# Kernel tuning notes

Hardware: AMD Instinct MI355X
Metric: run time of the kernel (lower is better)

The kernel has to match this reference:

```python
import jax, jax.numpy as jnp
import numpy as np

NC, NPER, DIN, D, R = 100000, 50000, 128, 128, 7
E = 2100000
ER = E // R  # edges per relation (block layout: relation i owns rows [i*ER, (i+1)*ER))
NEG_SLOPE = 0.2


def _seg_softmax(x, seg, n):
    # numerically-stable softmax over destination-node segments (PyG `softmax`)
    m = jax.ops.segment_max(x, seg, num_segments=n)
    m = jnp.where(jnp.isfinite(m), m, 0.0)  # empty segments -> -inf; neutralize
    e = jnp.exp(x - m[seg])
    s = jax.ops.segment_sum(e, seg, num_segments=n)
    return e / (s[seg] + 1e-16)


def setup_inputs() -> dict:
    key = jax.random.key(0)
    ks = jax.random.split(key, 12)
    N = NC + NPER
    s_in = 1.0 / float(np.sqrt(DIN))
    s_d = 1.0 / float(np.sqrt(D))
    company_emb = jax.random.normal(ks[0], (NC, DIN), jnp.float32)
    person_emb = jax.random.normal(ks[1], (NPER, DIN), jnp.float32)
    edge_index = jax.random.randint(ks[2], (E, 2), 0, N)
    edge_type = jnp.repeat(jnp.arange(R), ER)  # contiguous blocks per relation
    # weights are all-ones except relation 3 -> selects the weighted message branch there
    edge_weight = jnp.ones((E, 1), jnp.float32)
    edge_weight = edge_weight.at[3 * ER:4 * ER].set(
        jax.random.uniform(ks[3], (ER, 1), jnp.float32) + 0.1)
    W_com = jax.random.normal(ks[4], (DIN, D), jnp.float32) * s_in
    W_per = jax.random.normal(ks[5], (DIN, D), jnp.float32) * s_in
    Wq = jax.random.normal(ks[6], (R, D, D), jnp.float32) * s_d
    bq = jnp.zeros((R, D), jnp.float32)
    Wk = jax.random.normal(ks[7], (R, D, D), jnp.float32) * s_d
    bk = jnp.zeros((R, D), jnp.float32)
    Wv = jax.random.normal(ks[8], (D, D), jnp.float32) * s_d
    bv = jnp.zeros((D,), jnp.float32)
    pri = jnp.ones((R,), jnp.float32)
    W_rel_pair = jax.random.normal(ks[9], (R, 2 * D, D), jnp.float32) * s_d  # slot 3 unused
    W_rel3 = jax.random.normal(ks[10], (D, D), jnp.float32) * s_d
    skip = jnp.ones((1,), jnp.float32)
    return {"company_emb": company_emb, "person_emb": person_emb, "edge_weight": edge_weight,
            "W_com": W_com, "W_per": W_per, "Wq": Wq, "bq": bq, "Wk": Wk, "bk": bk,
            "Wv": Wv, "bv": bv, "pri": pri, "W_rel_pair": W_rel_pair, "W_rel3": W_rel3,
            "skip": skip, "edge_index": edge_index, "edge_type": edge_type}


def _hetegnn(company_emb, person_emb, edge_weight, W_com, W_per, Wq, bq, Wk, bk,
             Wv, bv, pri, W_rel_pair, W_rel3, skip, edge_index, edge_type):
    emb = jnp.concatenate([company_emb @ W_com, person_emb @ W_per], axis=0)  # [N, D]
    N = emb.shape[0]
    rs_list = []
    for i in range(R):
        sl = slice(i * ER, (i + 1) * ER)
        src = edge_index[sl, 0]
        dst = edge_index[sl, 1]
        x_j = emb[src]                                   # gathered source features [ER, D]
        if i == 3:  # weighted branch: linear on x_j, scalar scatter-softmax of edge weights
            msg = (x_j @ W_rel3) * _seg_softmax(edge_weight[sl], dst, N)
        else:       # attention branch: rel_wi(concat(x_i, x_j)) -> per-dim scatter-softmax
            temp = jnp.concatenate([emb[dst], x_j], axis=1) @ W_rel_pair[i]  # [ER, D]
            msg = x_j * _seg_softmax(temp, dst, N)
        rs = jax.ops.segment_sum(msg, dst, num_segments=N)  # scatter-add aggregation
        rs_list.append(jax.nn.leaky_relu(rs, NEG_SLOPE))
    rs_stack = jnp.stack(rs_list)                           # [R, N, D]
    # cross-relation attention
    q = jnp.einsum('nd,rde->rne', emb, Wq) + bq[:, None, :]
    k = jnp.einsum('rnd,rde->rne', rs_stack, Wk) + bk[:, None, :]
    scores = (q * k).sum(-1) * pri[:, None] / jnp.sqrt(jnp.float32(D))  # [R, N]
    att = jax.nn.softmax(scores, axis=0)                    # softmax across relations
    v = rs_stack @ Wv + bv                                  # [R, N, D]
    res = jnp.einsum('rn,rnd->nd', att, v)
    res = res + jax.nn.sigmoid(skip) * jax.nn.gelu(emb, approximate=False)
    return res


def reference(company_emb, person_emb, edge_weight, W_com, W_per, Wq, bq, Wk, bk,
              Wv, bv, pri, W_rel_pair, W_rel3, skip, edge_index, edge_type):
    res = _hetegnn(company_emb, person_emb, edge_weight, W_com, W_per, Wq, bq, Wk, bk,
                   Wv, bv, pri, W_rel_pair, W_rel3, skip, edge_index, edge_type)
    return res[:NC], res[NC:]
```

## Files before the change

### kernel.cpp

```cpp
#include <hip/hip_runtime.h>
#include <stdint.h>

#define NCY 100000
#define NPR 50000
#define NT  150000
#define RREL 7
#define ETOT 2100000
#define EREL 300000
#define NSEG (RREL*NT)
#define NEG 0.2f

#define NBUK 256
#define BWID 587
#define P1B  1024
#define CH1  2051
#define EPT  9
#define LSEG (RREL*BWID)
#define SPT  17

typedef __attribute__((ext_vector_type(8))) short short8;
typedef __attribute__((ext_vector_type(4))) float f32x4;
typedef unsigned short u16;

__device__ __forceinline__ float bf2f(u16 h){
  union{unsigned int u; float f;} v; v.u = ((unsigned int)h)<<16; return v.f;
}
__device__ __forceinline__ u16 f2bf(float f){
  union{unsigned int u; float f;} v; v.f=f;
  unsigned int u=v.u;
  return (u16)((u + 0x7fffu + ((u>>16)&1u))>>16);
}
__device__ __forceinline__ float lrelu(float x){ return x>0.f? x : NEG*x; }

#define MFMA(a,b,c) __builtin_amdgcn_mfma_f32_16x16x32_bf16(a,b,c,0,0,0)

__global__ __launch_bounds__(256) void k_bin(const int* __restrict__ eidx,
    const float* __restrict__ ew,
    int* __restrict__ bsrc, int* __restrict__ bkey, float* __restrict__ bew,
    int* __restrict__ gcntT, int* __restrict__ poffT){
  __shared__ int cnt[NBUK];
  __shared__ int pb[NBUK];
  int blk = blockIdx.x, tid = threadIdx.x;
  int base = blk*CH1;
  int n = min(CH1, ETOT-base);
  cnt[tid]=0;
  __syncthreads();
  int esrc[EPT], ekey[EPT], erank[EPT], ebuk[EPT]; float eew[EPT];
  #pragma unroll
  for(int k=0;k<EPT;k++){
    int i = k*256 + tid;
    erank[k]=-1; esrc[k]=0; ekey[k]=0; ebuk[k]=0; eew[k]=0.f;
    if(i<n){
      int e = base+i;
      int2 sd = *(const int2*)(eidx+2*e);
      int r = e/EREL;
      int b = sd.y / BWID;
      esrc[k]=sd.x; ekey[k]=r*NT+sd.y; ebuk[k]=b; eew[k]=ew[e];
      erank[k]=atomicAdd(&cnt[b],1);
    }
  }
  __syncthreads();
  int v = cnt[tid];
  pb[tid]=v; __syncthreads();
  for(int off=1; off<256; off<<=1){
    int a=(tid>=off)?pb[tid-off]:0; __syncthreads();
    pb[tid]+=a; __syncthreads();
  }
  int excl = pb[tid]-v;
  gcntT[blk*NBUK+tid]=v;
  poffT[blk*NBUK+tid]=excl;
  pb[tid]=excl; __syncthreads();
  #pragma unroll
  for(int k=0;k<EPT;k++){
    if(erank[k]>=0){
      int pos = base + pb[ebuk[k]] + erank[k];
      bsrc[pos]=esrc[k]; bkey[pos]=ekey[k]; bew[pos]=eew[k];
    }
  }
}

__global__ __launch_bounds__(256) void k_bsum(const int* __restrict__ gcntT,
                                              int* __restrict__ btot){
  __shared__ int lds[256];
  int b = blockIdx.x, t = threadIdx.x;
  int s=0;
  for(int blk=t; blk<P1B; blk+=256) s += gcntT[blk*NBUK+b];
  lds[t]=s; __syncthreads();
  for(int off=128; off>0; off>>=1){ if(t<off) lds[t]+=lds[t+off]; __syncthreads(); }
  if(t==0) btot[b]=lds[0];
}

__global__ __launch_bounds__(256) void k_bscan(const int* __restrict__ btot,
                                               int* __restrict__ bbase){
  __shared__ int lds[256];
  int t=threadIdx.x;
  int v=btot[t]; lds[t]=v; __syncthreads();
  for(int off=1; off<256; off<<=1){
    int a=(t>=off)?lds[t-off]:0; __syncthreads();
    lds[t]+=a; __syncthreads();
  }
  bbase[t]=lds[t]-v;
}

__global__ __launch_bounds__(256) void k_place(
    const int* __restrict__ bsrc, const int* __restrict__ bkey, const float* __restrict__ bew,
    const int* __restrict__ gcntT, const int* __restrict__ poffT, const int* __restrict__ bbase,
    int* __restrict__ starts_g, int* __restrict__ ends_g,
    int* __restrict__ ssrc, float* __restrict__ sew){
  __shared__ int scnt[LSEG];
  __shared__ int lrun[LSEG];
  __shared__ int gofs[P1B];
  __shared__ int gl[P1B];
  __shared__ int scan[256];
  int b = blockIdx.x, t = threadIdx.x;
  int lo = b*BWID;
  int gbase = bbase[b];
  for(int i=t;i<LSEG;i+=256) scnt[i]=0;
  for(int blk=t; blk<P1B; blk+=256){
    gl[blk]   = gcntT[blk*NBUK+b];
    gofs[blk] = poffT[blk*NBUK+b];
  }
  __syncthreads();
  for(int blk=t; blk<P1B; blk+=256){
    int o = blk*CH1 + gofs[blk], g = gl[blk];
    for(int i=0;i<g;i++){
      int key = bkey[o+i];
      int r = key/NT; int dst = key - r*NT;
      atomicAdd(&scnt[r*BWID + (dst-lo)], 1);
    }
  }
  __syncthreads();
  int ts=0;
  #pragma unroll
  for(int k=0;k<SPT;k++){ int idx=t*SPT+k; ts += (idx<LSEG)? scnt[idx]:0; }
  scan[t]=ts; __syncthreads();
  for(int off=1; off<256; off<<=1){
    int a=(t>=off)?scan[t-off]:0; __syncthreads();
    scan[t]+=a; __syncthreads();
  }
  int run = scan[t]-ts;
  #pragma unroll
  for(int k=0;k<SPT;k++){
    int idx=t*SPT+k;
    if(idx<LSEG){ lrun[idx]=run; run += scnt[idx]; }
  }
  __syncthreads();
  for(int idx=t; idx<LSEG; idx+=256){
    int r = idx/BWID; int ld = idx - r*BWID; int dst = lo+ld;
    if(dst<NT){
      int sgp = gbase + lrun[idx];
      starts_g[r*NT+dst] = sgp;
      ends_g[r*NT+dst]   = sgp + scnt[idx];
    }
  }
  __syncthreads();
  for(int idx=t; idx<LSEG; idx+=256) lrun[idx] += gbase;
  __syncthreads();
  for(int blk=t; blk<P1B; blk+=256){
    int o = blk*CH1 + gofs[blk], g = gl[blk];
    for(int i=0;i<g;i++){
      int key = bkey[o+i];
      int r = key/NT; int dst = key - r*NT;
      int pos = atomicAdd(&lrun[r*BWID+(dst-lo)], 1);
      ssrc[pos] = bsrc[o+i];
      if(r==3) sew[pos] = bew[o+i];
    }
  }
}

__global__ __launch_bounds__(256) void k_prep(const float* __restrict__ Wq, const float* __restrict__ bq,
    const float* __restrict__ Wk, const float* __restrict__ bk,
    float* __restrict__ Ar, float* __restrict__ ur, float* __restrict__ wr,
    float* __restrict__ cr, int* __restrict__ bflag){
  int t = blockIdx.x*256 + threadIdx.x;
  if(t >= RREL*128*128) return;
  int r = t/(128*128); int ij = t - r*128*128; int i = ij>>7, j = ij&127;
  const float* wq = Wq + r*16384; const float* wk = Wk + r*16384;
  float s=0.f;
  for(int k=0;k<128;k++) s += wq[i*128+k]*wk[j*128+k];
  Ar[t] = s;
  if(i==0){
    float su=0.f, sw=0.f;
    for(int k=0;k<128;k++){ su += wq[j*128+k]*bk[r*128+k];
                            sw += wk[j*128+k]*bq[r*128+k]; }
    ur[r*128+j]=su; wr[r*128+j]=sw;
    if(j==0){
      float sc=0.f; int nz=0;
      for(int k=0;k<128;k++){ float a=bq[r*128+k], b2=bk[r*128+k];
        sc += a*b2; nz |= (a!=0.f)||(b2!=0.f); }
      cr[r]=sc; if(nz) atomicOr(bflag,1);
    }
  }
}

struct PackJob{ const float* src; u16* dst; int ksteps; };
struct PackJobs{ PackJob j[20]; };
__global__ __launch_bounds__(256) void k_pack(PackJobs jobs){
  PackJob J = jobs.j[blockIdx.y];
  int t = blockIdx.x*256 + threadIdx.x;
  int lane = t&63, ks=(t>>6)&7, nt=t>>9;
  if(ks >= J.ksteps) return;
  int col = nt*16 + (lane&15);
  int krow = ks*32 + (lane>>4)*8;
  u16* d = J.dst + ((nt*J.ksteps + ks)*64 + lane)*8;
  for(int j=0;j<8;j++) d[j] = f2bf(J.src[(krow+j)*128 + col]);
}

struct GArgs {
  const void* A; const u16* B; int M; int rowoff;
  u16* outH; float* acc; float* den;
  const u16* emb16;
  const float* bv; const float* skip;
};

template<int EPI, int ASRC>
__global__ __launch_bounds__(256) void k_gemm(GArgs G)
{
  int wave = threadIdx.x>>6, lane = threadIdx.x&63;
  int M = G.M;
  int base = blockIdx.x*64 + wave*16;
  if(base >= M) return;
  int arow = base + (lane&15); if(arow >= M) arow = M-1;
  int kof = (lane>>4)*8;
  short8 a[4];
  if(ASRC==0){
    const u16* A = (const u16*)G.A;
    #pragma unroll
    for(int ks=0;ks<4;ks++) a[ks] = *(const short8*)(A + (size_t)arow*128 + ks*32 + kof);
  } else if(ASRC==3){
    const u16* A = (const u16*)G.A;
    float sc = 1.f/G.den[arow];
    #pragma unroll
    for(int ks=0;ks<4;ks++){
      short8 v = *(const short8*)(A + (size_t)arow*128 + ks*32 + kof);
      short8 s;
      #pragma unroll
      for(int j2=0;j2<8;j2++) s[j2]=f2bf(bf2f((u16)v[j2])*sc);
      a[ks]=s;
    }
  } else {
    const float* A = (const float*)G.A;
    #pragma unroll
    for(int ks=0;ks<4;ks++){
      const float* ap = A + (size_t)arow*128 + ks*32 + kof;
      f32x4 lo = *(const f32x4*)ap;
      f32x4 hi = *(const f32x4*)(ap+4);
      short8 s;
      #pragma unroll
      for(int j2=0;j2<4;j2++){ s[j2]=f2bf(lo[j2]); s[4+j2]=f2bf(hi[j2]); }
      a[ks]=s;
    }
  }
  f32x4 acc[8];
  #pragma unroll
  for(int nt=0;nt<8;nt++){
    f32x4 c = {0.f,0.f,0.f,0.f};
    #pragma unroll
    for(int ks=0;ks<4;ks++){
      short8 b = *(const short8*)(G.B + ((nt*4+ks)*64 + lane)*8);
      c = MFMA(a[ks], b, c);
    }
    acc[nt]=c;
  }
  int rbase = base + (lane>>4)*4;
  int cl = lane&15;
  if(EPI==0){
    #pragma unroll
    for(int nt=0;nt<8;nt++)
      for(int j=0;j<4;j++){
        int row=rbase+j;
        if(row<M){
          int col=nt*16+cl;
          G.outH[(size_t)(G.rowoff+row)*128+col] = f2bf(acc[nt][j]);
        }
      }
  } else if(EPI==1){
    #pragma unroll
    for(int nt=0;nt<8;nt++)
      for(int j=0;j<4;j++){
        int row=rbase+j;
        if(row<M){
          int col=nt*16+cl;
          G.outH[(size_t)row*128+col]=f2bf(lrelu(acc[nt][j]));
        }
      }
  } else {
    float sg = 1.f/(1.f+__expf(-G.skip[0]));
    #pragma unroll
    for(int nt=0;nt<8;nt++)
      for(int j=0;j<4;j++){
        int row=rbase+j;
        if(row<M){
          int col=nt*16+cl;
          float x = bf2f(G.emb16[(size_t)row*128+col]);
          float g = 0.5f*x*(1.f+erff(x*0.70710678118f));
          G.acc[(size_t)row*128+col] = acc[nt][j] + G.bv[col] + sg*g;
        }
      }
  }
}

struct FArgs {
  const u16* emb16; const u16* pA; const u16* pB2;
  const u16* rs; u16* acc16; float* den; u16* ebot;
  const float* uvec; const float* wvec; const float* cr; const int* bflag; const float* pri;
};

template<int HAS_EBOT>
__global__ __launch_bounds__(256) void k_facc(FArgs F)
{
  int wave = threadIdx.x>>6, lane = threadIdx.x&63;
  int base = blockIdx.x*64 + wave*16;
  if(base >= NT) return;
  int arow = base + (lane&15); if(arow >= NT) arow = NT-1;
  int kof = (lane>>4)*8;
  short8 a[4];
  #pragma unroll
  for(int ks=0;ks<4;ks++) a[ks] = *(const short8*)(F.emb16 + (size_t)arow*128 + ks*32 + kof);
  int rbase = base + (lane>>4)*4;
  int cl = lane&15;
  if(HAS_EBOT){
    #pragma unroll
    for(int nt=0;nt<8;nt++){
      f32x4 c = {0.f,0.f,0.f,0.f};
      #pragma unroll
      for(int ks=0;ks<4;ks++){
        short8 b = *(const short8*)(F.pB2 + ((nt*4+ks)*64 + lane)*8);
        c = MFMA(a[ks], b, c);
      }
      #pragma unroll
      for(int j=0;j<4;j++){
        int row=rbase+j;
        if(row<NT) F.ebot[(size_t)row*128 + nt*16+cl] = f2bf(__expf(c[j]));
      }
    }
  }
  f32x4 accS[8];
  #pragma unroll
  for(int nt=0;nt<8;nt++){
    f32x4 c = {0.f,0.f,0.f,0.f};
    #pragma unroll
    for(int ks=0;ks<4;ks++){
      short8 b = *(const short8*)(F.pA + ((nt*4+ks)*64 + lane)*8);
      c = MFMA(a[ks], b, c);
    }
    accS[nt]=c;
  }
  float prival = F.pri[0] * 0.08838834764831845f;
  int bias = *F.bflag;
  float rsv[4][8];
  #pragma unroll
  for(int j=0;j<4;j++){
    int row=rbase+j; bool ok = row<NT;
    #pragma unroll
    for(int nt=0;nt<8;nt++){
      int col=nt*16+cl;
      rsv[j][nt] = ok ? bf2f(F.rs[(size_t)row*128+col]) : 0.f;
    }
  }
  #pragma unroll
  for(int j=0;j<4;j++){
    int row=rbase+j; bool ok = row<NT;
    float p=0.f;
    if(ok){
      #pragma unroll
      for(int nt=0;nt<8;nt++) p += accS[nt][j]*rsv[j][nt];
      if(bias){
        #pragma unroll
        for(int nt=0;nt<8;nt++){
          int col=nt*16+cl;
          p += bf2f(F.emb16[(size_t)row*128+col])*F.uvec[col]
             + rsv[j][nt]*F.wvec[col];
        }
      }
    }
    p += __shfl_xor(p,1,16); p += __shfl_xor(p,2,16);
    p += __shfl_xor(p,4,16); p += __shfl_xor(p,8,16);
    float e = __expf((p + F.cr[0])*prival);
    if(ok){
      #pragma unroll
      for(int nt=0;nt<8;nt++){
        size_t o=(size_t)row*128 + nt*16+cl;
        F.acc16[o] = f2bf(bf2f(F.acc16[o]) + e*rsv[j][nt]);
      }
      if(cl==0) F.den[row] += e;
    }
  }
}

__global__ __launch_bounds__(256) void k_edge2s(const u16* __restrict__ ebot,
    const u16* __restrict__ emb16, const int* __restrict__ ssrc,
    const int* __restrict__ starts_g, const int* __restrict__ ends_g, int rel,
    u16* __restrict__ rsout){
  int n = blockIdx.x*16 + (threadIdx.x>>4);
  int dof = (threadIdx.x&15)*8;
  int s = starts_g[rel*NT + n];
  int e_end = ends_g[rel*NT + n];
  float num[8]={0,0,0,0,0,0,0,0}, den[8]={0,0,0,0,0,0,0,0};
  int p = s;
  for(; p+1 < e_end; p += 2){
    int s0 = ssrc[p], s1 = ssrc[p+1];
    short8 ev0 = *(const short8*)(ebot  + (size_t)s0*128 + dof);
    short8 xj0 = *(const short8*)(emb16 + (size_t)s0*128 + dof);
    short8 ev1 = *(const short8*)(ebot  + (size_t)s1*128 + dof);
    short8 xj1 = *(const short8*)(emb16 + (size_t)s1*128 + dof);
    #pragma unroll
    for(int j=0;j<8;j++){
      float e0 = bf2f((u16)ev0[j]), e1 = bf2f((u16)ev1[j]);
      num[j] += bf2f((u16)xj0[j])*e0 + bf2f((u16)xj1[j])*e1;
      den[j] += e0 + e1;
    }
  }
  if(p < e_end){
    int s0 = ssrc[p];
    short8 ev0 = *(const short8*)(ebot  + (size_t)s0*128 + dof);
    short8 xj0 = *(const short8*)(emb16 + (size_t)s0*128 + dof);
    #pragma unroll
    for(int j=0;j<8;j++){
      float e0 = bf2f((u16)ev0[j]);
      num[j] += bf2f((u16)xj0[j])*e0;
      den[j] += e0;
    }
  }
  u16 o8[8];
  #pragma unroll
  for(int j=0;j<8;j++) o8[j] = f2bf(lrelu(num[j]/(den[j]+1e-16f)));
  *(short8*)(rsout + (size_t)n*128 + dof) = *(short8*)o8;
}

__global__ __launch_bounds__(256) void k_rel3s(const float* __restrict__ sew,
    const u16* __restrict__ emb16, const int* __restrict__ ssrc,
    const int* __restrict__ starts_g, const int* __restrict__ ends_g,
    u16* __restrict__ t16){
  int n = blockIdx.x*16 + (threadIdx.x>>4);
  int dof = (threadIdx.x&15)*8;
  int s = starts_g[3*NT + n];
  int e_end = ends_g[3*NT + n];
  float num[8]={0,0,0,0,0,0,0,0}, den=0.f;
  for(int p=s; p<e_end; p++){
    int src = ssrc[p];
    float wv = __expf(sew[p]);
    den += wv;
    short8 xj8 = *(const short8*)(emb16 + (size_t)src*128 + dof);
    #pragma unroll
    for(int j=0;j<8;j++) num[j] += wv*bf2f((u16)xj8[j]);
  }
  float inv = 1.f/(den+1e-16f);
  u16 o8[8];
  #pragma unroll
  for(int j=0;j<8;j++) o8[j] = f2bf(num[j]*inv);
  *(short8*)(t16 + (size_t)n*128 + dof) = *(short8*)o8;
}

extern "C" void kernel_launch(void* const* d_in, const int* in_sizes, int n_in,
                              void* d_out, int out_size, void* d_ws, size_t ws_size,
                              hipStream_t stream){
  const float* company = (const float*)d_in[0];
  const float* person  = (const float*)d_in[1];
  const float* eweight = (const float*)d_in[2];
  const float* W_com   = (const float*)d_in[3];
  const float* W_per   = (const float*)d_in[4];
  const float* Wq      = (const float*)d_in[5];
  const float* bq      = (const float*)d_in[6];
  const float* Wk      = (const float*)d_in[7];
  const float* bk      = (const float*)d_in[8];
  const float* Wv      = (const float*)d_in[9];
  const float* bvv     = (const float*)d_in[10];
  const float* pri     = (const float*)d_in[11];
  const float* Wpair   = (const float*)d_in[12];
  const float* Wrel3   = (const float*)d_in[13];
  const float* skip    = (const float*)d_in[14];
  const int*   eidx    = (const int*)d_in[15];
  float* out = (float*)d_out;

  char* w = (char*)d_ws;
  auto alloc = [&](size_t sz)->void*{ void* p=(void*)w; w += (sz+255)&~(size_t)255; return p; };
  u16*   emb16 = (u16*)alloc((size_t)NT*128*2);
  u16*   ebot  = (u16*)alloc((size_t)NT*128*2);
  u16*   rs16  = (u16*)alloc((size_t)NT*128*2);
  u16*   acc16 = (u16*)alloc((size_t)NT*128*2);
  float* den   = (float*)alloc((size_t)NT*4);
  int*   starts_g = (int*)alloc((size_t)NSEG*4);
  int*   ends_g   = (int*)alloc((size_t)NSEG*4);
  int*   ssrc  = (int*)alloc((size_t)ETOT*4);
  float* sew   = (float*)alloc((size_t)ETOT*4);
  float* Ar    = (float*)alloc((size_t)RREL*16384*4);
  float* ur    = (float*)alloc(RREL*128*4);
  float* wr    = (float*)alloc(RREL*128*4);
  float* cr    = (float*)alloc(RREL*4);
  int*   bflag = (int*)alloc(256);
  u16* pWcom  = (u16*)alloc(16384*2);
  u16* pWper  = (u16*)alloc(16384*2);
  u16* pWrel3 = (u16*)alloc(16384*2);
  u16* pWv    = (u16*)alloc(16384*2);
  u16* pAr    = (u16*)alloc((size_t)RREL*16384*2);
  u16* pWbot  = (u16*)alloc((size_t)6*16384*2);
  (void)ws_size; (void)in_sizes; (void)n_in; (void)out_size;

  int*   bsrc  = (int*)rs16;
  int*   bkey  = bsrc + ETOT;
  float* bew   = (float*)(bkey + ETOT);
  int*   gcntT = (int*)acc16;
  int*   poffT = gcntT + P1B*NBUK;
  int*   btot  = poffT + P1B*NBUK;
  int*   bbase = btot + NBUK;

  hipMemsetAsync(den, 0, (size_t)NT*4, stream);
  hipMemsetAsync(bflag, 0, 4, stream);

  k_bin<<<P1B,256,0,stream>>>(eidx, eweight, bsrc, bkey, bew, gcntT, poffT);
  k_bsum<<<NBUK,256,0,stream>>>(gcntT, btot);
  k_bscan<<<1,256,0,stream>>>(btot, bbase);
  k_place<<<NBUK,256,0,stream>>>(bsrc,bkey,bew,gcntT,poffT,bbase,
                                 starts_g,ends_g,ssrc,sew);
  hipMemsetAsync(acc16, 0, (size_t)NT*128*2, stream);

  k_prep<<<(RREL*16384+255)/256,256,0,stream>>>(Wq,bq,Wk,bk,Ar,ur,wr,cr,bflag);

  const int attr[6] = {0,1,2,4,5,6};
  PackJobs pj{};
  int nj=0;
  auto addjob=[&](const float* s,u16* d,int ks){ pj.j[nj].src=s; pj.j[nj].dst=d; pj.j[nj].ksteps=ks; nj++; };
  addjob(W_com,pWcom,4); addjob(W_per,pWper,4);
  addjob(Wrel3,pWrel3,4); addjob(Wv,pWv,4);
  for(int r=0;r<RREL;r++) addjob(Ar + (size_t)r*16384, pAr + (size_t)r*16384, 4);
  for(int i=0;i<6;i++) addjob(Wpair + (size_t)attr[i]*32768 + 16384, pWbot + (size_t)i*16384, 4);
  dim3 pg(16, nj);
  k_pack<<<pg,256,0,stream>>>(pj);

  GArgs g{};
  g = GArgs{}; g.A=company; g.B=pWcom; g.M=NCY; g.rowoff=0; g.outH=emb16;
  k_gemm<0,1><<<(NCY+63)/64,256,0,stream>>>(g);
  g = GArgs{}; g.A=person; g.B=pWper; g.M=NPR; g.rowoff=NCY; g.outH=emb16;
  k_gemm<0,1><<<(NPR+63)/64,256,0,stream>>>(g);

  auto facc = [&](int r, int ebslot){
    FArgs f{};
    f.emb16=emb16; f.pA=pAr+(size_t)r*16384; f.rs=rs16; f.acc16=acc16; f.den=den;
    f.uvec=ur+(size_t)r*128; f.wvec=wr+(size_t)r*128; f.cr=cr+r; f.bflag=bflag; f.pri=pri+r;
    if(ebslot>=0){
      f.pB2=pWbot+(size_t)ebslot*16384; f.ebot=ebot;
      k_facc<1><<<(NT+63)/64,256,0,stream>>>(f);
    } else {
      k_facc<0><<<(NT+63)/64,256,0,stream>>>(f);
    }
  };

  k_rel3s<<<NT/16,256,0,stream>>>(sew,emb16,ssrc,starts_g,ends_g,ebot);
  g = GArgs{}; g.A=ebot; g.B=pWrel3; g.M=NT; g.outH=rs16;
  k_gemm<1,0><<<(NT+63)/64,256,0,stream>>>(g);
  facc(3, 0);

  for(int i=0;i<6;i++){
    int r = attr[i];
    k_edge2s<<<NT/16,256,0,stream>>>(ebot,emb16,ssrc,starts_g,ends_g,r, rs16);
    facc(r, (i<5)? i+1 : -1);
  }

  g = GArgs{}; g.A=acc16; g.B=pWv; g.M=NT;
  g.acc=out; g.den=den; g.emb16=emb16; g.bv=bvv; g.skip=skip;
  k_gemm<3,3><<<(NT+63)/64,256,0,stream>>>(g);
}
```

Before: 957.9 us.

## Fuse edge gather with attention accumulation, processing two relations per kernel

Replaces the separate per-relation edge-gather kernel and attention-accumulate kernel with fused kernels. Each block gathers segment-softmax messages for 64 nodes into LDS and then runs the MFMA scoring and accumulation from LDS. Relations are processed in pairs, so each launch computes exp tables for the next two relations and the acc16/den read-modify-write runs half as often. Relation 3's gather and its W_rel3 GEMM are fused as well. This removes the rs16 round trips and about ten launches. The cost is double-buffered exp tables stored in the output buffer, more LDS per block, and a gather pattern of one thread per 16 columns that may lower memory-level parallelism.

```diff
diff --git a/kernel.cpp b/kernel.cpp
--- a/kernel.cpp
+++ b/kernel.cpp
@@ -17,6 +17,8 @@
 #define EPT  9
 #define LSEG (RREL*BWID)
 #define SPT  17
+
+#define LSTR 136
 
 typedef __attribute__((ext_vector_type(8))) short short8;
 typedef __attribute__((ext_vector_type(4))) float f32x4;
@@ -274,14 +276,14 @@
           G.outH[(size_t)(G.rowoff+row)*128+col] = f2bf(acc[nt][j]);
         }
       }
-  } else if(EPI==1){
+  } else if(EPI==4){
     #pragma unroll
     for(int nt=0;nt<8;nt++)
       for(int j=0;j<4;j++){
         int row=rbase+j;
         if(row<M){
           int col=nt*16+cl;
-          G.outH[(size_t)row*128+col]=f2bf(lrelu(acc[nt][j]));
+          G.outH[(size_t)row*128+col]=f2bf(__expf(acc[nt][j]));
         }
       }
   } else {
@@ -300,156 +302,366 @@
   }
 }
 
-struct FArgs {
-  const u16* emb16; const u16* pA; const u16* pB2;
-  const u16* rs; u16* acc16; float* den; u16* ebot;
-  const float* uvec; const float* wvec; const float* cr; const int* bflag; const float* pri;
+struct PArgs {
+  const u16* emb16; const int* ssrc; const int* starts_g; const int* ends_g;
+  const float* sew;
+  const u16* ebR1; const u16* ebR2;
+  const u16* pA1; const u16* pA2;
+  const u16* pWr3;
+  const u16* pB2a; const u16* pB2b; u16* ebW1; u16* ebW2;
+  u16* acc16; float* den;
+  const float* u1; const float* w1; const float* c1; const float* p1;
+  const float* u2; const float* w2; const float* c2; const float* p2;
+  const int* bflag;
+  int r1, r2;
 };
 
-template<int HAS_EBOT>
-__global__ __launch_bounds__(256) void k_facc(FArgs F)
+__device__ __forceinline__ void gatherAtt(u16* buf, const u16* __restrict__ ebt,
+    const u16* __restrict__ emb16, const int* __restrict__ ssrc,
+    const int* __restrict__ sg, const int* __restrict__ eg,
+    int rel, int base64, int tid){
+  #pragma unroll
+  for(int p2=0;p2<2;p2++){
+    int ln = (tid>>3) + p2*32;
+    int gn = base64 + ln;
+    int cb = (tid&7)*16;
+    float num[16]={0,0,0,0,0,0,0,0,0,0,0,0,0,0,0,0};
+    float den[16]={0,0,0,0,0,0,0,0,0,0,0,0,0,0,0,0};
+    if(gn<NT){
+      int s=sg[rel*NT+gn], e=eg[rel*NT+gn];
+      for(int pos=s;pos<e;pos++){
+        int src=ssrc[pos];
+        const u16* eb=ebt+(size_t)src*128+cb;
+        const u16* xm=emb16+(size_t)src*128+cb;
+        short8 e0=*(const short8*)eb, e1=*(const short8*)(eb+8);
+        short8 x0=*(const short8*)xm, x1=*(const short8*)(xm+8);
+        #pragma unroll
+        for(int j=0;j<8;j++){
+          float ev0=bf2f((u16)e0[j]), ev1=bf2f((u16)e1[j]);
+          num[j]   += bf2f((u16)x0[j])*ev0; den[j]   += ev0;
+          num[8+j] += bf2f((u16)x1[j])*ev1; den[8+j] += ev1;
+        }
+      }
+    }
+    #pragma unroll
+    for(int j=0;j<16;j++) buf[ln*LSTR+cb+j] = f2bf(lrelu(num[j]/(den[j]+1e-16f)));
+  }
+}
+
+__device__ __forceinline__ void gatherR3(u16* buf, const float* __restrict__ sew,
+    const u16* __restrict__ emb16, const int* __restrict__ ssrc,
+    const int* __restrict__ sg, const int* __restrict__ eg,
+    int base64, int tid){
+  #pragma unroll
+  for(int p2=0;p2<2;p2++){
+    int ln = (tid>>3) + p2*32;
+    int gn = base64 + ln;
+    int cb = (tid&7)*16;
+    float num[16]={0,0,0,0,0,0,0,0,0,0,0,0,0,0,0,0};
+    float dn=0.f;
+    if(gn<NT){
+      int s=sg[3*NT+gn], e=eg[3*NT+gn];
+      for(int pos=s;pos<e;pos++){
+        int src=ssrc[pos];
+        float wv=__expf(sew[pos]);
+        dn += wv;
+        const u16* xm=emb16+(size_t)src*128+cb;
+        short8 x0=*(const short8*)xm, x1=*(const short8*)(xm+8);
+        #pragma unroll
+        for(int j=0;j<8;j++){
+          num[j]   += wv*bf2f((u16)x0[j]);
+          num[8+j] += wv*bf2f((u16)x1[j]);
+        }
+      }
+    }
+    float inv=1.f/(dn+1e-16f);
+    #pragma unroll
+    for(int j=0;j<16;j++) buf[ln*LSTR+cb+j] = f2bf(num[j]*inv);
+  }
+}
+
+template<int NR, int NEB>
+__global__ __launch_bounds__(256) void k_fp(PArgs P)
 {
-  int wave = threadIdx.x>>6, lane = threadIdx.x&63;
-  int base = blockIdx.x*64 + wave*16;
+  __shared__ u16 lds1[64*LSTR];
+  __shared__ u16 lds2[64*LSTR];
+  int tid = threadIdx.x;
+  int base64 = blockIdx.x*64;
+  gatherAtt(lds1, P.ebR1, P.emb16, P.ssrc, P.starts_g, P.ends_g, P.r1, base64, tid);
+  if(NR==2) gatherAtt(lds2, P.ebR2, P.emb16, P.ssrc, P.starts_g, P.ends_g, P.r2, base64, tid);
+  __syncthreads();
+  int wave=tid>>6, lane=tid&63;
+  int base = base64 + wave*16;
   if(base >= NT) return;
   int arow = base + (lane&15); if(arow >= NT) arow = NT-1;
   int kof = (lane>>4)*8;
   short8 a[4];
   #pragma unroll
-  for(int ks=0;ks<4;ks++) a[ks] = *(const short8*)(F.emb16 + (size_t)arow*128 + ks*32 + kof);
+  for(int ks=0;ks<4;ks++) a[ks] = *(const short8*)(P.emb16 + (size_t)arow*128 + ks*32 + kof);
   int rbase = base + (lane>>4)*4;
+  int lrb   = wave*16 + (lane>>4)*4;
   int cl = lane&15;
-  if(HAS_EBOT){
+  int bias = *P.bflag;
+  float e1v[4], e2v[4];
+  {
+    f32x4 accS[8];
     #pragma unroll
     for(int nt=0;nt<8;nt++){
       f32x4 c = {0.f,0.f,0.f,0.f};
       #pragma unroll
       for(int ks=0;ks<4;ks++){
-        short8 b = *(const short8*)(F.pB2 + ((nt*4+ks)*64 + lane)*8);
+        short8 b = *(const short8*)(P.pA1 + ((nt*4+ks)*64 + lane)*8);
         c = MFMA(a[ks], b, c);
       }
-      #pragma unroll
-      for(int j=0;j<4;j++){
-        int row=rbase+j;
-        if(row<NT) F.ebot[(size_t)row*128 + nt*16+cl] = f2bf(__expf(c[j]));
-      }
-    }
-  }
-  f32x4 accS[8];
-  #pragma unroll
-  for(int nt=0;nt<8;nt++){
-    f32x4 c = {0.f,0.f,0.f,0.f};
-    #pragma unroll
-    for(int ks=0;ks<4;ks++){
-      short8 b = *(const short8*)(F.pA + ((nt*4+ks)*64 + lane)*8);
-      c = MFMA(a[ks], b, c);
-    }
-    accS[nt]=c;
-  }
-  float prival = F.pri[0] * 0.08838834764831845f;
-  int bias = *F.bflag;
-  float rsv[4][8];
-  #pragma unroll
-  for(int j=0;j<4;j++){
-    int row=rbase+j; bool ok = row<NT;
-    #pragma unroll
-    for(int nt=0;nt<8;nt++){
-      int col=nt*16+cl;
-      rsv[j][nt] = ok ? bf2f(F.rs[(size_t)row*128+col]) : 0.f;
-    }
-  }
-  #pragma unroll
-  for(int j=0;j<4;j++){
-    int row=rbase+j; bool ok = row<NT;
-    float p=0.f;
-    if(ok){
-      #pragma unroll
-      for(int nt=0;nt<8;nt++) p += accS[nt][j]*rsv[j][nt];
-      if(bias){
+      accS[nt]=c;
+    }
+    float prival = P.p1[0]*0.08838834764831845f;
+    #pragma unroll
+    for(int j=0;j<4;j++){
+      int row=rbase+j; bool ok=row<NT;
+      float p=0.f;
+      if(ok){
         #pragma unroll
         for(int nt=0;nt<8;nt++){
           int col=nt*16+cl;
-          p += bf2f(F.emb16[(size_t)row*128+col])*F.uvec[col]
-             + rsv[j][nt]*F.wvec[col];
-        }
-      }
-    }
-    p += __shfl_xor(p,1,16); p += __shfl_xor(p,2,16);
-    p += __shfl_xor(p,4,16); p += __shfl_xor(p,8,16);
-    float e = __expf((p + F.cr[0])*prival);
-    if(ok){
+          float rv = bf2f(lds1[(lrb+j)*LSTR+col]);
+          p += accS[nt][j]*rv;
+          if(bias) p += bf2f(P.emb16[(size_t)row*128+col])*P.u1[col] + rv*P.w1[col];
+        }
+      }
+      p += __shfl_xor(p,1,16); p += __shfl_xor(p,2,16);
+      p += __shfl_xor(p,4,16); p += __shfl_xor(p,8,16);
+      e1v[j] = __expf((p + P.c1[0])*prival);
+    }
+  }
+  if(NR==2){
+    f32x4 accS[8];
+    #pragma unroll
+    for(int nt=0;nt<8;nt++){
+      f32x4 c = {0.f,0.f,0.f,0.f};
+      #pragma unroll
+      for(int ks=0;ks<4;ks++){
+        short8 b = *(const short8*)(P.pA2 + ((nt*4+ks)*64 + lane)*8);
+        c = MFMA(a[ks], b, c);
+      }
+      accS[nt]=c;
+    }
+    float prival = P.p2[0]*0.08838834764831845f;
+    #pragma unroll
+    for(int j=0;j<4;j++){
+      int row=rbase+j; bool ok=row<NT;
+      float p=0.f;
+      if(ok){
+        #pragma unroll
+        for(int nt=0;nt<8;nt++){
+          int col=nt*16+cl;
+          float rv = bf2f(lds2[(lrb+j)*LSTR+col]);
+          p += accS[nt][j]*rv;
+          if(bias) p += bf2f(P.emb16[(size_t)row*128+col])*P.u2[col] + rv*P.w2[col];
+        }
+      }
+      p += __shfl_xor(p,1,16); p += __shfl_xor(p,2,16);
+      p += __shfl_xor(p,4,16); p += __shfl_xor(p,8,16);
+      e2v[j] = __expf((p + P.c2[0])*prival);
+    }
+  }
+  #pragma unroll
+  for(int j=0;j<4;j++){
+    int row=rbase+j;
+    if(row<NT){
+      float ee1=e1v[j];
+      float ee2=(NR==2)? e2v[j] : 0.f;
       #pragma unroll
       for(int nt=0;nt<8;nt++){
-        size_t o=(size_t)row*128 + nt*16+cl;
-        F.acc16[o] = f2bf(bf2f(F.acc16[o]) + e*rsv[j][nt]);
-      }
-      if(cl==0) F.den[row] += e;
-    }
-  }
-}
-
-__global__ __launch_bounds__(256) void k_edge2s(const u16* __restrict__ ebot,
-    const u16* __restrict__ emb16, const int* __restrict__ ssrc,
-    const int* __restrict__ starts_g, const int* __restrict__ ends_g, int rel,
-    u16* __restrict__ rsout){
-  int n = blockIdx.x*16 + (threadIdx.x>>4);
-  int dof = (threadIdx.x&15)*8;
-  int s = starts_g[rel*NT + n];
-  int e_end = ends_g[rel*NT + n];
-  float num[8]={0,0,0,0,0,0,0,0}, den[8]={0,0,0,0,0,0,0,0};
-  int p = s;
-  for(; p+1 < e_end; p += 2){
-    int s0 = ssrc[p], s1 = ssrc[p+1];
-    short8 ev0 = *(const short8*)(ebot  + (size_t)s0*128 + dof);
-    short8 xj0 = *(const short8*)(emb16 + (size_t)s0*128 + dof);
-    short8 ev1 = *(const short8*)(ebot  + (size_t)s1*128 + dof);
-    short8 xj1 = *(const short8*)(emb16 + (size_t)s1*128 + dof);
-    #pragma unroll
-    for(int j=0;j<8;j++){
-      float e0 = bf2f((u16)ev0[j]), e1 = bf2f((u16)ev1[j]);
-      num[j] += bf2f((u16)xj0[j])*e0 + bf2f((u16)xj1[j])*e1;
-      den[j] += e0 + e1;
-    }
-  }
-  if(p < e_end){
-    int s0 = ssrc[p];
-    short8 ev0 = *(const short8*)(ebot  + (size_t)s0*128 + dof);
-    short8 xj0 = *(const short8*)(emb16 + (size_t)s0*128 + dof);
-    #pragma unroll
-    for(int j=0;j<8;j++){
-      float e0 = bf2f((u16)ev0[j]);
-      num[j] += bf2f((u16)xj0[j])*e0;
-      den[j] += e0;
-    }
-  }
-  u16 o8[8];
-  #pragma unroll
-  for(int j=0;j<8;j++) o8[j] = f2bf(lrelu(num[j]/(den[j]+1e-16f)));
-  *(short8*)(rsout + (size_t)n*128 + dof) = *(short8*)o8;
-}
-
-__global__ __launch_bounds__(256) void k_rel3s(const float* __restrict__ sew,
-    const u16* __restrict__ emb16, const int* __restrict__ ssrc,
-    const int* __restrict__ starts_g, const int* __restrict__ ends_g,
-    u16* __restrict__ t16){
-  int n = blockIdx.x*16 + (threadIdx.x>>4);
-  int dof = (threadIdx.x&15)*8;
-  int s = starts_g[3*NT + n];
-  int e_end = ends_g[3*NT + n];
-  float num[8]={0,0,0,0,0,0,0,0}, den=0.f;
-  for(int p=s; p<e_end; p++){
-    int src = ssrc[p];
-    float wv = __expf(sew[p]);
-    den += wv;
-    short8 xj8 = *(const short8*)(emb16 + (size_t)src*128 + dof);
-    #pragma unroll
-    for(int j=0;j<8;j++) num[j] += wv*bf2f((u16)xj8[j]);
-  }
-  float inv = 1.f/(den+1e-16f);
-  u16 o8[8];
-  #pragma unroll
-  for(int j=0;j<8;j++) o8[j] = f2bf(num[j]*inv);
-  *(short8*)(t16 + (size_t)n*128 + dof) = *(short8*)o8;
+        int col=nt*16+cl;
+        size_t o=(size_t)row*128+col;
+        float add = ee1*bf2f(lds1[(lrb+j)*LSTR+col]);
+        if(NR==2) add += ee2*bf2f(lds2[(lrb+j)*LSTR+col]);
+        P.acc16[o] = f2bf(bf2f(P.acc16[o]) + add);
+      }
+      if(cl==0) P.den[row] += ee1 + ee2;
+    }
+  }
+  if(NEB>=1){
+    #pragma unroll
+    for(int nt=0;nt<8;nt++){
+      f32x4 c = {0.f,0.f,0.f,0.f};
+      #pragma unroll
+      for(int ks=0;ks<4;ks++){
+        short8 b = *(const short8*)(P.pB2a + ((nt*4+ks)*64 + lane)*8);
+        c = MFMA(a[ks], b, c);
+      }
+      #pragma unroll
+      for(int j=0;j<4;j++){
+        int row=rbase+j;
+        if(row<NT) P.ebW1[(size_t)row*128 + nt*16+cl] = f2bf(__expf(c[j]));
+      }
+    }
+  }
+  if(NEB>=2){
+    #pragma unroll
+    for(int nt=0;nt<8;nt++){
+      f32x4 c = {0.f,0.f,0.f,0.f};
+      #pragma unroll
+      for(int ks=0;ks<4;ks++){
+        short8 b = *(const short8*)(P.pB2b + ((nt*4+ks)*64 + lane)*8);
+        c = MFMA(a[ks], b, c);
+      }
+      #pragma unroll
+      for(int j=0;j<4;j++){
+        int row=rbase+j;
+        if(row<NT) P.ebW2[(size_t)row*128 + nt*16+cl] = f2bf(__expf(c[j]));
+      }
+    }
+  }
+}
+
+__global__ __launch_bounds__(256) void k_fp0(PArgs P)
+{
+  __shared__ u16 lds1[64*LSTR];
+  __shared__ u16 lds2[64*LSTR];
+  int tid = threadIdx.x;
+  int base64 = blockIdx.x*64;
+  gatherR3(lds1, P.sew, P.emb16, P.ssrc, P.starts_g, P.ends_g, base64, tid);
+  gatherAtt(lds2, P.ebR2, P.emb16, P.ssrc, P.starts_g, P.ends_g, P.r2, base64, tid);
+  __syncthreads();
+  int wave=tid>>6, lane=tid&63;
+  int base = base64 + wave*16;
+  if(base >= NT) return;
+  int arow = base + (lane&15); if(arow >= NT) arow = NT-1;
+  int kof = (lane>>4)*8;
+  int lar = wave*16 + (lane&15);
+  short8 a[4];
+  #pragma unroll
+  for(int ks=0;ks<4;ks++) a[ks] = *(const short8*)(P.emb16 + (size_t)arow*128 + ks*32 + kof);
+  f32x4 rs3[8];
+  {
+    short8 ta[4];
+    #pragma unroll
+    for(int ks=0;ks<4;ks++) ta[ks] = *(const short8*)(lds1 + lar*LSTR + ks*32 + kof);
+    #pragma unroll
+    for(int nt=0;nt<8;nt++){
+      f32x4 c = {0.f,0.f,0.f,0.f};
+      #pragma unroll
+      for(int ks=0;ks<4;ks++){
+        short8 b = *(const short8*)(P.pWr3 + ((nt*4+ks)*64 + lane)*8);
+        c = MFMA(ta[ks], b, c);
+      }
+      #pragma unroll
+      for(int j=0;j<4;j++) c[j] = lrelu(c[j]);
+      rs3[nt]=c;
+    }
+  }
+  int rbase = base + (lane>>4)*4;
+  int lrb   = wave*16 + (lane>>4)*4;
+  int cl = lane&15;
+  int bias = *P.bflag;
+  float e1v[4], e2v[4];
+  {
+    f32x4 accS[8];
+    #pragma unroll
+    for(int nt=0;nt<8;nt++){
+      f32x4 c = {0.f,0.f,0.f,0.f};
+      #pragma unroll
+      for(int ks=0;ks<4;ks++){
+        short8 b = *(const short8*)(P.pA1 + ((nt*4+ks)*64 + lane)*8);
+        c = MFMA(a[ks], b, c);
+      }
+      accS[nt]=c;
+    }
+    float prival = P.p1[0]*0.08838834764831845f;
+    #pragma unroll
+    for(int j=0;j<4;j++){
+      int row=rbase+j; bool ok=row<NT;
+      float p=0.f;
+      if(ok){
+        #pragma unroll
+        for(int nt=0;nt<8;nt++){
+          int col=nt*16+cl;
+          float rv = rs3[nt][j];
+          p += accS[nt][j]*rv;
+          if(bias) p += bf2f(P.emb16[(size_t)row*128+col])*P.u1[col] + rv*P.w1[col];
+        }
+      }
+      p += __shfl_xor(p,1,16); p += __shfl_xor(p,2,16);
+      p += __shfl_xor(p,4,16); p += __shfl_xor(p,8,16);
+      e1v[j] = __expf((p + P.c1[0])*prival);
+    }
+  }
+  {
+    f32x4 accS[8];
+    #pragma unroll
+    for(int nt=0;nt<8;nt++){
+      f32x4 c = {0.f,0.f,0.f,0.f};
+      #pragma unroll
+      for(int ks=0;ks<4;ks++){
+        short8 b = *(const short8*)(P.pA2 + ((nt*4+ks)*64 + lane)*8);
+        c = MFMA(a[ks], b, c);
+      }
+      accS[nt]=c;
+    }
+    float prival = P.p2[0]*0.08838834764831845f;
+    #pragma unroll
+    for(int j=0;j<4;j++){
+      int row=rbase+j; bool ok=row<NT;
+      float p=0.f;
+      if(ok){
+        #pragma unroll
+        for(int nt=0;nt<8;nt++){
+          int col=nt*16+cl;
+          float rv = bf2f(lds2[(lrb+j)*LSTR+col]);
+          p += accS[nt][j]*rv;
+          if(bias) p += bf2f(P.emb16[(size_t)row*128+col])*P.u2[col] + rv*P.w2[col];
+        }
+      }
+      p += __shfl_xor(p,1,16); p += __shfl_xor(p,2,16);
+      p += __shfl_xor(p,4,16); p += __shfl_xor(p,8,16);
+      e2v[j] = __expf((p + P.c2[0])*prival);
+    }
+  }
+  #pragma unroll
+  for(int j=0;j<4;j++){
+    int row=rbase+j;
+    if(row<NT){
+      float ee1=e1v[j], ee2=e2v[j];
+      #pragma unroll
+      for(int nt=0;nt<8;nt++){
+        int col=nt*16+cl;
+        size_t o=(size_t)row*128+col;
+        float add = ee1*bf2f(f2bf(rs3[nt][j])) + ee2*bf2f(lds2[(lrb+j)*LSTR+col]);
+        P.acc16[o] = f2bf(bf2f(P.acc16[o]) + add);
+      }
+      if(cl==0) P.den[row] += ee1 + ee2;
+    }
+  }
+  #pragma unroll
+  for(int nt=0;nt<8;nt++){
+    f32x4 c = {0.f,0.f,0.f,0.f};
+    #pragma unroll
+    for(int ks=0;ks<4;ks++){
+      short8 b = *(const short8*)(P.pB2a + ((nt*4+ks)*64 + lane)*8);
+      c = MFMA(a[ks], b, c);
+    }
+    #pragma unroll
+    for(int j=0;j<4;j++){
+      int row=rbase+j;
+      if(row<NT) P.ebW1[(size_t)row*128 + nt*16+cl] = f2bf(__expf(c[j]));
+    }
+  }
+  #pragma unroll
+  for(int nt=0;nt<8;nt++){
+    f32x4 c = {0.f,0.f,0.f,0.f};
+    #pragma unroll
+    for(int ks=0;ks<4;ks++){
+      short8 b = *(const short8*)(P.pB2b + ((nt*4+ks)*64 + lane)*8);
+      c = MFMA(a[ks], b, c);
+    }
+    #pragma unroll
+    for(int j=0;j<4;j++){
+      int row=rbase+j;
+      if(row<NT) P.ebW2[(size_t)row*128 + nt*16+cl] = f2bf(__expf(c[j]));
+    }
+  }
 }
 
 extern "C" void kernel_launch(void* const* d_in, const int* in_sizes, int n_in,
@@ -476,8 +688,8 @@
   char* w = (char*)d_ws;
   auto alloc = [&](size_t sz)->void*{ void* p=(void*)w; w += (sz+255)&~(size_t)255; return p; };
   u16*   emb16 = (u16*)alloc((size_t)NT*128*2);
-  u16*   ebot  = (u16*)alloc((size_t)NT*128*2);
-  u16*   rs16  = (u16*)alloc((size_t)NT*128*2);
+  u16*   ebA   = (u16*)alloc((size_t)NT*128*2);
+  u16*   ebB   = (u16*)alloc((size_t)NT*128*2);
   u16*   acc16 = (u16*)alloc((size_t)NT*128*2);
   float* den   = (float*)alloc((size_t)NT*4);
   int*   starts_g = (int*)alloc((size_t)NSEG*4);
@@ -497,7 +709,10 @@
   u16* pWbot  = (u16*)alloc((size_t)6*16384*2);
   (void)ws_size; (void)in_sizes; (void)n_in; (void)out_size;
 
-  int*   bsrc  = (int*)rs16;
+  u16* ebC = (u16*)d_out;
+  u16* ebD = ebC + (size_t)NT*128;
+
+  int*   bsrc  = (int*)ebA;
   int*   bkey  = bsrc + ETOT;
   float* bew   = (float*)(bkey + ETOT);
   int*   gcntT = (int*)acc16;
@@ -534,28 +749,31 @@
   g = GArgs{}; g.A=person; g.B=pWper; g.M=NPR; g.rowoff=NCY; g.outH=emb16;
   k_gemm<0,1><<<(NPR+63)/64,256,0,stream>>>(g);
 
-  auto facc = [&](int r, int ebslot){
-    FArgs f{};
-    f.emb16=emb16; f.pA=pAr+(size_t)r*16384; f.rs=rs16; f.acc16=acc16; f.den=den;
-    f.uvec=ur+(size_t)r*128; f.wvec=wr+(size_t)r*128; f.cr=cr+r; f.bflag=bflag; f.pri=pri+r;
-    if(ebslot>=0){
-      f.pB2=pWbot+(size_t)ebslot*16384; f.ebot=ebot;
-      k_facc<1><<<(NT+63)/64,256,0,stream>>>(f);
-    } else {
-      k_facc<0><<<(NT+63)/64,256,0,stream>>>(f);
-    }
+  g = GArgs{}; g.A=emb16; g.B=pWbot; g.M=NT; g.outH=ebA;
+  k_gemm<4,0><<<(NT+63)/64,256,0,stream>>>(g);
+
+  int NBLK = (NT+63)/64;
+  auto mkP = [&](int r1,int r2,const u16* eb1,const u16* eb2,
+                 int sa,int sb,u16* w1,u16* w2)->PArgs{
+    PArgs P{};
+    P.emb16=emb16; P.ssrc=ssrc; P.starts_g=starts_g; P.ends_g=ends_g; P.sew=sew;
+    P.ebR1=eb1; P.ebR2=eb2;
+    P.pA1=pAr+(size_t)r1*16384; P.pA2=pAr+(size_t)r2*16384;
+    P.pWr3=pWrel3;
+    P.pB2a=(sa>=0)? pWbot+(size_t)sa*16384 : nullptr;
+    P.pB2b=(sb>=0)? pWbot+(size_t)sb*16384 : nullptr;
+    P.ebW1=w1; P.ebW2=w2;
+    P.acc16=acc16; P.den=den;
+    P.u1=ur+(size_t)r1*128; P.w1=wr+(size_t)r1*128; P.c1=cr+r1; P.p1=pri+r1;
+    P.u2=ur+(size_t)r2*128; P.w2=wr+(size_t)r2*128; P.c2=cr+r2; P.p2=pri+r2;
+    P.bflag=bflag; P.r1=r1; P.r2=r2;
+    return P;
   };
 
-  k_rel3s<<<NT/16,256,0,stream>>>(sew,emb16,ssrc,starts_g,ends_g,ebot);
-  g = GArgs{}; g.A=ebot; g.B=pWrel3; g.M=NT; g.outH=rs16;
-  k_gemm<1,0><<<(NT+63)/64,256,0,stream>>>(g);
-  facc(3, 0);
-
-  for(int i=0;i<6;i++){
-    int r = attr[i];
-    k_edge2s<<<NT/16,256,0,stream>>>(ebot,emb16,ssrc,starts_g,ends_g,r, rs16);
-    facc(r, (i<5)? i+1 : -1);
-  }
+  k_fp0<<<NBLK,256,0,stream>>>(mkP(3,0, nullptr,ebA, 1,2, ebC,ebD));
+  k_fp<2,2><<<NBLK,256,0,stream>>>(mkP(1,2, ebC,ebD, 3,4, ebA,ebB));
+  k_fp<2,1><<<NBLK,256,0,stream>>>(mkP(4,5, ebA,ebB, 5,-1, ebC,nullptr));
+  k_fp<1,0><<<NBLK,256,0,stream>>>(mkP(6,6, ebC,nullptr, -1,-1, nullptr,nullptr));
 
   g = GArgs{}; g.A=acc16; g.B=pWv; g.M=NT;
   g.acc=out; g.den=den; g.emb16=emb16; g.bv=bvv; g.skip=skip;
```

New measurement: 904.9 us. 5.5% less time.
